# Kernel optimization log

Hardware: AMD Instinct MI355X
Metric: run time of the kernel (lower is better)

## Reference

```python
import jax, jax.numpy as jnp
import numpy as np
from math import sqrt

B, S, D_MODEL, H, DK, DV = 16, 512, 256, 8, 32, 32
EPS = 1e-5


def layer_norm(x, g, b):
    m = jnp.mean(x, axis=-1, keepdims=True)
    v = jnp.mean((x - m) ** 2, axis=-1, keepdims=True)
    return g * (x - m) / jnp.sqrt(v + EPS) + b


def setup_inputs() -> dict:
    key = jax.random.key(0)
    ks = jax.random.split(key, 16)
    inp = {
        "input_Q": jax.random.normal(ks[0], (B, S, D_MODEL), jnp.float32),
        "input_K": jax.random.normal(ks[1], (B, S, D_MODEL), jnp.float32),
        "input_V": jax.random.normal(ks[2], (B, S, D_MODEL), jnp.float32),
        "attn_mask": jax.random.bernoulli(ks[3], 0.1, (B, H, S, S)),
        "matrix": jax.random.uniform(ks[4], (B, S, S), jnp.float32),
        # learned params (stored [in, out], i.e. transpose of torch Linear weight)
        "W_Q": jax.random.normal(ks[5], (D_MODEL, H * DK), jnp.float32) * 0.02,
        "W_K": jax.random.normal(ks[6], (D_MODEL, H * DK), jnp.float32) * 0.02,
        "W_V": jax.random.normal(ks[7], (D_MODEL, H * DV), jnp.float32) * 0.02,
        "W_V2": jax.random.normal(ks[8], (D_MODEL, DV), jnp.float32) * 0.02,
        "W_fc": jax.random.normal(ks[9], (DV * (H + 1), D_MODEL), jnp.float32) * 0.02,
        "ln_g": jnp.ones((D_MODEL,), jnp.float32),
        "ln_b": jnp.zeros((D_MODEL,), jnp.float32),
        "fu_ln_g": jnp.ones((H + 1,), jnp.float32),
        "fu_ln_b": jnp.zeros((H + 1,), jnp.float32),
        "fu_w1": jax.random.normal(ks[10], (H + 1, 6), jnp.float32) * 0.3,
        "fu_b1": jnp.zeros((6,), jnp.float32),
        "fu_w2": jax.random.normal(ks[11], (6, 1), jnp.float32) * 0.3,
        "fu_b2": jnp.zeros((1,), jnp.float32),
    }
    return inp


def reference(input_Q, input_K, input_V, attn_mask, matrix,
              W_Q, W_K, W_V, W_V2, W_fc, ln_g, ln_b,
              fu_ln_g, fu_ln_b, fu_w1, fu_b1, fu_w2, fu_b2):
    b = input_Q.shape[0]
    # project and split heads: [B, H, S, d]
    Q = (input_Q @ W_Q).reshape(b, -1, H, DK).transpose(0, 2, 1, 3)
    K = (input_K @ W_K).reshape(b, -1, H, DK).transpose(0, 2, 1, 3)
    V = (input_V @ W_V).reshape(b, -1, H, DV).transpose(0, 2, 1, 3)
    scores = jnp.einsum('bhqd,bhkd->bhqk', Q, K) / sqrt(DK)
    scores = jnp.where(attn_mask, -1e9, scores)
    attn = jax.nn.softmax(scores, axis=-1)            # [B, H, S, S]
    context = jnp.einsum('bhqk,bhkd->bhqd', attn, V)  # [B, H, S, DV]
    # second context from pairwise matrix
    context2 = matrix @ (input_V @ W_V2)              # [B, S, DV]
    # gated matrix update: concat matrix with attn maps along head axis
    gate_in = jnp.concatenate([matrix[:, None], attn], axis=1)  # [B, H+1, S, S]
    gate_in = gate_in.transpose(0, 3, 2, 1)                     # [B, S, S, H+1]
    g = layer_norm(gate_in, fu_ln_g, fu_ln_b)
    g = jax.nn.relu(g @ fu_w1 + fu_b1)
    g = jax.nn.sigmoid(g @ fu_w2 + fu_b2)[..., 0]               # [B, S, S]
    matrix_out = matrix * g
    # merge heads, concat, project, layernorm
    context = context.transpose(0, 2, 1, 3).reshape(b, -1, H * DV)
    context = jnp.concatenate([context, context2], axis=-1)     # [B, S, DV*(H+1)]
    output = layer_norm(context @ W_fc, ln_g, ln_b)
    return (output, matrix_out)
```

## Files before the change

kernel.cpp:

```cpp
#include <hip/hip_runtime.h>
#include <hip/hip_bf16.h>

#define BB 16
#define SS 512
#define DM 256
#define NH 8

#define OFF_QB    0
#define OFF_KB    1048576
#define OFF_VT    2097152
#define OFF_VP2   3145728
#define OFF_CTXB  3407872
#define OFF_CTX2B 4456448
#define OFF_G     4587520
#define OFF_FLAG  6684672
#define OFF_PM    6684674

#define SCALE 0.17677669529663687f
#define KE2 0.2550348623f

typedef __attribute__((ext_vector_type(8))) short bfrag8;
typedef __attribute__((ext_vector_type(4))) float facc4;

__global__ void mask_or_kernel(const unsigned int* __restrict__ w,
                               unsigned int* __restrict__ acc) {
  __shared__ unsigned int sh[256];
  unsigned int a = 0;
  int base = blockIdx.x * 1024;
  for (int i = threadIdx.x; i < 1024; i += 256) a |= w[base + i];
  sh[threadIdx.x] = a;
  __syncthreads();
  for (int s = 128; s > 0; s >>= 1) {
    if (threadIdx.x < s) sh[threadIdx.x] |= sh[threadIdx.x + s];
    __syncthreads();
  }
  if (threadIdx.x == 0) atomicOr(acc, sh[0]);
}

__global__ __launch_bounds__(256) void mask_pack_kernel(
    const void* __restrict__ mask, unsigned long long* __restrict__ pm,
    const unsigned int* __restrict__ orv) {
  const unsigned int rawor = *orv;
  const int flagv = (rawor <= 1u) ? 0 : ((rawor == 0x3F800000u) ? 2 : 1);
  const int lane = threadIdx.x & 63;
  const int wv = threadIdx.x >> 6;
  const int w0 = (blockIdx.x * 4 + wv) * 32;
  const unsigned char* mb = (const unsigned char*)mask;
  const int* mi = (const int*)mask;
  const float* mf = (const float*)mask;
  unsigned long long myw = 0;
#pragma unroll 4
  for (int i = 0; i < 32; i++) {
    long long idx = (long long)(w0 + i) * 64 + lane;
    bool m;
    if (flagv == 1) m = (mb[idx] != 0);
    else if (flagv == 0) m = (mi[idx] != 0);
    else m = (mf[idx] != 0.f);
    unsigned long long bits = __ballot(m);
    if (lane == i) myw = bits;
  }
  if (lane < 32) pm[w0 + lane] = myw;
}

__global__ __launch_bounds__(256) void proj_pack_kernel(
    const float* __restrict__ inQ, const float* __restrict__ inK,
    const float* __restrict__ inV,
    const float* __restrict__ Wq, const float* __restrict__ Wk,
    const float* __restrict__ Wv, const float* __restrict__ Wv2,
    __hip_bfloat16* __restrict__ Qb, __hip_bfloat16* __restrict__ Kb,
    __hip_bfloat16* __restrict__ Vt, float* __restrict__ Vp2,
    const unsigned int* __restrict__ mask4,
    unsigned long long* __restrict__ pm) {
  __shared__ __align__(16) char smem[16640];
  const int tid = threadIdx.x;

  if (blockIdx.x < 1536) {
    auto As = reinterpret_cast<__hip_bfloat16(*)[40]>(smem);
    auto Bs = reinterpret_cast<__hip_bfloat16(*)[40]>(smem + 5120);
    const int bid = blockIdx.x;
    const int matid = bid >> 9;
    const int mblk = (bid & 511) >> 2;
    const int nblk = bid & 3;
    const int m0 = mblk * 64;
    const int n0 = nblk * 64;
    const float* X = (matid == 0) ? inQ : (matid == 1) ? inK : inV;
    const float* W = (matid == 0) ? Wq : (matid == 1) ? Wk : Wv;

    const int lane = tid & 63;
    const int w = tid >> 6;
    const int wm = w & 1, wn = w >> 1;
    const int cl = lane & 15, quad = lane >> 4;
    const int arow = tid >> 2, ak8 = (tid & 3) * 8;
    const int bn = tid & 63, bk8 = (tid >> 6) * 8;

    facc4 acc[2][2];
#pragma unroll
    for (int t = 0; t < 2; t++)
#pragma unroll
      for (int u = 0; u < 2; u++) acc[t][u] = (facc4){0.f, 0.f, 0.f, 0.f};

#pragma unroll 1
    for (int kc = 0; kc < 8; kc++) {
      float4 x0 = *(const float4*)&X[(m0 + arow) * 256 + kc * 32 + ak8];
      float4 x1 = *(const float4*)&X[(m0 + arow) * 256 + kc * 32 + ak8 + 4];
      float wv[8];
#pragma unroll
      for (int j = 0; j < 8; j++)
        wv[j] = W[(kc * 32 + bk8 + j) * 256 + n0 + bn];
      __syncthreads();
      {
        __hip_bfloat16 ta[8];
        ta[0] = __float2bfloat16(x0.x); ta[1] = __float2bfloat16(x0.y);
        ta[2] = __float2bfloat16(x0.z); ta[3] = __float2bfloat16(x0.w);
        ta[4] = __float2bfloat16(x1.x); ta[5] = __float2bfloat16(x1.y);
        ta[6] = __float2bfloat16(x1.z); ta[7] = __float2bfloat16(x1.w);
        *(uint4*)&As[arow][ak8] = *(uint4*)ta;
        __hip_bfloat16 tb[8];
#pragma unroll
        for (int j = 0; j < 8; j++) tb[j] = __float2bfloat16(wv[j]);
        *(uint4*)&Bs[bn][bk8] = *(uint4*)tb;
      }
      __syncthreads();
      bfrag8 aA[2], bB[2];
#pragma unroll
      for (int t = 0; t < 2; t++)
        aA[t] = *(const bfrag8*)&As[wm * 32 + t * 16 + cl][quad * 8];
#pragma unroll
      for (int u = 0; u < 2; u++)
        bB[u] = *(const bfrag8*)&Bs[wn * 32 + u * 16 + cl][quad * 8];
#pragma unroll
      for (int t = 0; t < 2; t++)
#pragma unroll
        for (int u = 0; u < 2; u++)
          acc[t][u] = __builtin_amdgcn_mfma_f32_16x16x32_bf16(aA[t], bB[u],
                                                             acc[t][u], 0, 0, 0);
    }

    if (matid < 2) {
      __hip_bfloat16* Y = (matid == 0) ? Qb : Kb;
#pragma unroll
      for (int t = 0; t < 2; t++)
#pragma unroll
        for (int u = 0; u < 2; u++)
#pragma unroll
          for (int reg = 0; reg < 4; reg++)
            Y[(m0 + wm * 32 + t * 16 + quad * 4 + reg) * 256 + n0 + wn * 32 +
              u * 16 + cl] = __float2bfloat16(acc[t][u][reg]);
    } else {
#pragma unroll
      for (int t = 0; t < 2; t++)
#pragma unroll
        for (int u = 0; u < 2; u++) {
          int c = n0 + wn * 32 + u * 16 + cl;
          int mg = m0 + wm * 32 + t * 16 + quad * 4;
          int b = mg >> 9, s = mg & 511;
          __hip_bfloat16 pk[4];
#pragma unroll
          for (int reg = 0; reg < 4; reg++)
            pk[reg] = __float2bfloat16(acc[t][u][reg]);
          *(ushort4*)&Vt[(((b << 8) + c) << 9) + s] = *(ushort4*)pk;
        }
    }
  } else if (blockIdx.x < 2048) {
    auto xs = reinterpret_cast<float(*)[260]>(smem);
    const int r0 = (blockIdx.x - 1536) * 16;
    for (int e = tid; e < 16 * 256; e += 256) {
      int r = e >> 8, i = e & 255;
      xs[r][i] = inV[(r0 + r) * 256 + i];
    }
    __syncthreads();
    const int c2 = tid & 31, rr = tid >> 5;
    float a0 = 0.f, a1 = 0.f;
    for (int i = 0; i < 256; i += 4) {
      float w0 = Wv2[i * 32 + c2], w1 = Wv2[(i + 1) * 32 + c2];
      float w2 = Wv2[(i + 2) * 32 + c2], w3 = Wv2[(i + 3) * 32 + c2];
      float4 xa = *(const float4*)&xs[rr][i];
      float4 xb = *(const float4*)&xs[rr + 8][i];
      a0 += xa.x * w0 + xa.y * w1 + xa.z * w2 + xa.w * w3;
      a1 += xb.x * w0 + xb.y * w1 + xb.z * w2 + xb.w * w3;
    }
    Vp2[(r0 + rr) * 32 + c2] = a0;
    Vp2[(r0 + rr + 8) * 32 + c2] = a1;
  } else {
    const int lane = tid & 63;
    const int wv = tid >> 6;
    const int w0 = ((blockIdx.x - 2048) * 4 + wv) * 32;
    unsigned long long myw = 0;
#pragma unroll 4
    for (int i = 0; i < 32; i++) {
      unsigned int v = mask4[(long long)(w0 + i) * 64 + lane];
      unsigned long long bits = __ballot(v != 0u);
      if (lane == i) myw = bits;
    }
    if (lane < 32) pm[w0 + lane] = myw;
  }
}

__global__ __launch_bounds__(512, 2) void attn_kernel(
    const __hip_bfloat16* __restrict__ Qb, const __hip_bfloat16* __restrict__ Kb,
    const __hip_bfloat16* __restrict__ Vt,
    const unsigned long long* __restrict__ pm,
    const float* __restrict__ matrix,
    const float* __restrict__ fulng, const float* __restrict__ fulnb,
    const float* __restrict__ fuw1, const float* __restrict__ fub1,
    const float* __restrict__ fuw2, const float* __restrict__ fub2,
    __hip_bfloat16* __restrict__ ctxb, __hip_bfloat16* __restrict__ gws) {
  __shared__ __align__(16) __hip_bfloat16 Sb[NH][16][520];
  __shared__ float inv_s[NH][16];
  __shared__ float gp[80];

  const int tid = threadIdx.x;
  const int lane = tid & 63;
  const int h = tid >> 6;
  const int cl = lane & 15, quad = lane >> 4;
  const int b = ((blockIdx.x & 7) << 1) | (blockIdx.x >> 8);
  const int q0 = ((blockIdx.x >> 3) & 31) * 16;

  if (tid < 6) {
    const int j = tid;
    float s1 = 0.f, c1 = fub1[j];
#pragma unroll
    for (int t = 0; t < 9; t++) {
      float w = fuw1[t * 6 + j];
      float gw = fulng[t] * w;
      gp[t * 6 + j] = gw;
      s1 += gw;
      c1 += fulnb[t] * w;
    }
    gp[54 + j] = s1;
    gp[60 + j] = c1;
    gp[66 + j] = fuw2[j];
    if (j == 0) gp[72] = fub2[0];
  }

  const unsigned long long* pmb = pm + (((b * NH + h) << 9) + q0) * 8;

  const bfrag8 aQ =
      *(const bfrag8*)&Qb[(((b << 9) + q0 + cl) << 8) + h * 32 + quad * 8];
  const __hip_bfloat16* KbB = &Kb[((b << 9) << 8) + h * 32 + quad * 8];
  const __hip_bfloat16* VtB = &Vt[(((b << 8) + h * 32) << 9)];

  float l[4] = {0.f, 0.f, 0.f, 0.f};
#pragma unroll 2
  for (int w8 = 0; w8 < 8; w8++) {
    unsigned long long mw[4];
#pragma unroll
    for (int r = 0; r < 4; r++)
      mw[r] = pmb[(quad * 4 + r) * 8 + w8] >> cl;
#pragma unroll
    for (int n4 = 0; n4 < 4; n4++) {
      const int nt = w8 * 4 + n4;
      bfrag8 bK = *(const bfrag8*)&KbB[(nt * 16 + cl) << 8];
      facc4 cc = {0.f, 0.f, 0.f, 0.f};
      cc = __builtin_amdgcn_mfma_f32_16x16x32_bf16(aQ, bK, cc, 0, 0, 0);
#pragma unroll
      for (int r = 0; r < 4; r++) {
        float e = ((mw[r] >> (n4 * 16)) & 1ULL) ? 0.f : exp2f(KE2 * cc[r]);
        l[r] += e;
        Sb[h][quad * 4 + r][nt * 16 + cl] = __float2bfloat16(e);
      }
    }
  }
#pragma unroll
  for (int r = 0; r < 4; r++)
#pragma unroll
    for (int off = 1; off <= 8; off <<= 1) l[r] += __shfl_xor(l[r], off);
  float invl[4];
#pragma unroll
  for (int r = 0; r < 4; r++) invl[r] = 1.f / l[r];
  if (cl == 0) {
#pragma unroll
    for (int r = 0; r < 4; r++) inv_s[h][quad * 4 + r] = invl[r];
  }
  __syncthreads();

  facc4 a0 = {0.f, 0.f, 0.f, 0.f}, a1 = {0.f, 0.f, 0.f, 0.f};
#pragma unroll 4
  for (int ks = 0; ks < 16; ks++) {
    bfrag8 aP = *(const bfrag8*)&Sb[h][cl][ks * 32 + quad * 8];
    bfrag8 b0 = *(const bfrag8*)&VtB[(cl << 9) + ks * 32 + quad * 8];
    bfrag8 b1 = *(const bfrag8*)&VtB[((16 + cl) << 9) + ks * 32 + quad * 8];
    a0 = __builtin_amdgcn_mfma_f32_16x16x32_bf16(aP, b0, a0, 0, 0, 0);
    a1 = __builtin_amdgcn_mfma_f32_16x16x32_bf16(aP, b1, a1, 0, 0, 0);
  }

  {
    const int gq = tid >> 5;
    const int g32 = (tid & 31) * 4;
#pragma unroll 1
    for (int s = 0; s < 4; s++) {
      const int k4 = s * 128 + g32;
      float4 mrow =
          *(const float4*)&matrix[((b << 9) + q0 + gq) * 512 + k4];
      float p[NH][4];
#pragma unroll
      for (int hh = 0; hh < NH; hh++) {
        const float iv = inv_s[hh][gq];
        ushort4 sv = *(const ushort4*)&Sb[hh][gq][k4];
        p[hh][0] = __bfloat162float(*(__hip_bfloat16*)&sv.x) * iv;
        p[hh][1] = __bfloat162float(*(__hip_bfloat16*)&sv.y) * iv;
        p[hh][2] = __bfloat162float(*(__hip_bfloat16*)&sv.z) * iv;
        p[hh][3] = __bfloat162float(*(__hip_bfloat16*)&sv.w) * iv;
      }
      const float mcomp[4] = {mrow.x, mrow.y, mrow.z, mrow.w};
      __hip_bfloat16 gout[4];
#pragma unroll
      for (int i = 0; i < 4; i++) {
        float v[9];
        v[0] = mcomp[i];
#pragma unroll
        for (int t = 0; t < NH; t++) v[1 + t] = p[t][i];
        float s1 = 0.f, s2 = 0.f;
#pragma unroll
        for (int t = 0; t < 9; t++) {
          s1 += v[t];
          s2 += v[t] * v[t];
        }
        float mu = s1 * (1.f / 9.f);
        float var = s2 * (1.f / 9.f) - mu * mu;
        float inv = rsqrtf(var + 1e-5f);
        float o = gp[72];
#pragma unroll
        for (int j = 0; j < 6; j++) {
          float d = 0.f;
#pragma unroll
          for (int t = 0; t < 9; t++) d += v[t] * gp[t * 6 + j];
          float z = inv * (d - mu * gp[54 + j]) + gp[60 + j];
          z = fmaxf(z, 0.f);
          o += z * gp[66 + j];
        }
        gout[i] = __float2bfloat16(1.f / (1.f + __expf(-o)));
      }
      *(ushort4*)&gws[((b << 9) + q0 + gq) * 512 + k4] = *(ushort4*)gout;
    }
  }

#pragma unroll
  for (int r = 0; r < 4; r++) {
    int row = quad * 4 + r;
    ctxb[((b << 9) + q0 + row) * 256 + h * 32 + cl] =
        __float2bfloat16(a0[r] * invl[r]);
    ctxb[((b << 9) + q0 + row) * 256 + h * 32 + 16 + cl] =
        __float2bfloat16(a1[r] * invl[r]);
  }
}

__global__ __launch_bounds__(256) void mout_ctx2_kernel(
    const float* __restrict__ matrix, const __hip_bfloat16* __restrict__ g,
    float* __restrict__ mout, const float* __restrict__ Vp2,
    __hip_bfloat16* __restrict__ ctx2b) {
  __shared__ __align__(16) char smem[25088];
  const int tid = threadIdx.x;

  if (blockIdx.x < 1024) {
    auto Gs = reinterpret_cast<float(*)[65]>(smem);
    const int b = blockIdx.x >> 6;
    const int j0 = ((blockIdx.x >> 3) & 7) * 64;
    const int i0 = (blockIdx.x & 7) * 64;

    {
      int r = tid >> 2, c0 = (tid & 3) * 16;
      const __hip_bfloat16* gpx = g + (((b << 9) + i0 + r) << 9) + j0 + c0;
      ushort us[16];
      *(uint4*)(us) = *(const uint4*)(gpx);
      *(uint4*)(us + 8) = *(const uint4*)(gpx + 8);
#pragma unroll
      for (int k = 0; k < 16; k++) {
        __hip_bfloat16 hv = *(__hip_bfloat16*)&us[k];
        Gs[r][c0 + k] = __bfloat162float(hv);
      }
    }
    __syncthreads();

    {
      int jj = tid >> 2, ic = (tid & 3) * 16;
      const float* mp = matrix + (((b << 9) + j0 + jj) << 9) + i0 + ic;
      float* op = mout + (((b << 9) + j0 + jj) << 9) + i0 + ic;
#pragma unroll
      for (int v4 = 0; v4 < 4; v4++) {
        float4 m = *(const float4*)(mp + v4 * 4);
        float4 o;
        o.x = m.x * Gs[ic + v4 * 4 + 0][jj];
        o.y = m.y * Gs[ic + v4 * 4 + 1][jj];
        o.z = m.z * Gs[ic + v4 * 4 + 2][jj];
        o.w = m.w * Gs[ic + v4 * 4 + 3][jj];
        *(float4*)(op + v4 * 4) = o;
      }
    }
  } else {
    auto Ms = reinterpret_cast<float(*)[128]>(smem);
    auto Vs2t = reinterpret_cast<float(*)[132]>(smem + 8192);
    const int cid = blockIdx.x - 1024;
    const int b = cid >> 5;
    const int s0 = (cid & 31) * 16;
    const int dv = tid & 31, rg = tid >> 5;
    float acc0 = 0.f, acc1 = 0.f;
    for (int kc = 0; kc < 4; kc++) {
      __syncthreads();
#pragma unroll
      for (int it = 0; it < 8; it++) {
        int idx = tid + it * 256;
        int r = idx >> 7, cc = idx & 127;
        Ms[r][cc] = matrix[((b << 9) + s0 + r) * 512 + kc * 128 + cc];
      }
#pragma unroll
      for (int it = 0; it < 16; it++) {
        int e = tid + it * 256;
        int k = e >> 5, dv2 = e & 31;
        Vs2t[dv2][k] = Vp2[((b << 9) + kc * 128 + k) * 32 + dv2];
      }
      __syncthreads();
      for (int k = 0; k < 128; k += 4) {
        float4 vv = *(const float4*)&Vs2t[dv][k];
        float4 m0 = *(const float4*)&Ms[rg][k];
        float4 m1 = *(const float4*)&Ms[rg + 8][k];
        acc0 += m0.x * vv.x + m0.y * vv.y + m0.z * vv.z + m0.w * vv.w;
        acc1 += m1.x * vv.x + m1.y * vv.y + m1.z * vv.z + m1.w * vv.w;
      }
    }
    ctx2b[((b << 9) + s0 + rg) * 32 + dv] = __float2bfloat16(acc0);
    ctx2b[((b << 9) + s0 + rg + 8) * 32 + dv] = __float2bfloat16(acc1);
  }
}

__global__ __launch_bounds__(256) void final_kernel(
    const __hip_bfloat16* __restrict__ ctxb,
    const __hip_bfloat16* __restrict__ ctx2b, const float* __restrict__ Wfc,
    const float* __restrict__ lng, const float* __restrict__ lnb,
    float* __restrict__ out) {
  __shared__ __align__(16) __hip_bfloat16 As[32][40];
  __shared__ __align__(16) __hip_bfloat16 Bs[256][40];
  __shared__ __align__(16) float xs[32][260];
  __shared__ float red2[32][8][2];
  __shared__ float musig[32][2];
  const int tid = threadIdx.x;
  const int m0 = blockIdx.x * 32;
  const int lane = tid & 63, w = tid >> 6;
  const int cl = lane & 15, quad = lane >> 4;
  const int arow = tid >> 3, ak4 = (tid & 7) * 4;

  facc4 acc[2][4];
#pragma unroll
  for (int t = 0; t < 2; t++)
#pragma unroll
    for (int u = 0; u < 4; u++) acc[t][u] = (facc4){0.f, 0.f, 0.f, 0.f};

#pragma unroll 1
  for (int kc = 0; kc < 9; kc++) {
    ushort4 av;
    if (kc < 8)
      av = *(const ushort4*)&ctxb[(m0 + arow) * 256 + kc * 32 + ak4];
    else
      av = *(const ushort4*)&ctx2b[(m0 + arow) * 32 + ak4];
    float wv[32];
#pragma unroll
    for (int j = 0; j < 32; j++) wv[j] = Wfc[(kc * 32 + j) * 256 + tid];
    __syncthreads();
    *(ushort4*)&As[arow][ak4] = av;
    {
      __hip_bfloat16 tw[32];
#pragma unroll
      for (int j = 0; j < 32; j++) tw[j] = __float2bfloat16(wv[j]);
#pragma unroll
      for (int g = 0; g < 4; g++) *(uint4*)&Bs[tid][g * 8] = *(uint4*)&tw[g * 8];
    }
    __syncthreads();
    bfrag8 aA[2], bB[4];
#pragma unroll
    for (int t = 0; t < 2; t++)
      aA[t] = *(const bfrag8*)&As[t * 16 + cl][quad * 8];
#pragma unroll
    for (int u = 0; u < 4; u++)
      bB[u] = *(const bfrag8*)&Bs[w * 64 + u * 16 + cl][quad * 8];
#pragma unroll
    for (int t = 0; t < 2; t++)
#pragma unroll
      for (int u = 0; u < 4; u++)
        acc[t][u] =
            __builtin_amdgcn_mfma_f32_16x16x32_bf16(aA[t], bB[u], acc[t][u], 0, 0, 0);
  }

#pragma unroll
  for (int t = 0; t < 2; t++)
#pragma unroll
    for (int u = 0; u < 4; u++)
#pragma unroll
      for (int reg = 0; reg < 4; reg++)
        xs[t * 16 + quad * 4 + reg][w * 64 + u * 16 + cl] = acc[t][u][reg];
  __syncthreads();

  {
    int r = tid >> 3, c0 = (tid & 7) * 32;
    float s1 = 0.f, s2 = 0.f;
    for (int j = 0; j < 32; j += 4) {
      float4 v = *(const float4*)&xs[r][c0 + j];
      s1 += v.x + v.y + v.z + v.w;
      s2 += v.x * v.x + v.y * v.y + v.z * v.z + v.w * v.w;
    }
    red2[r][tid & 7][0] = s1;
    red2[r][tid & 7][1] = s2;
  }
  __syncthreads();
  if (tid < 32) {
    float s1 = 0.f, s2 = 0.f;
#pragma unroll
    for (int j = 0; j < 8; j++) {
      s1 += red2[tid][j][0];
      s2 += red2[tid][j][1];
    }
    float mu = s1 * (1.f / 256.f);
    float var = s2 * (1.f / 256.f) - mu * mu;
    musig[tid][0] = mu;
    musig[tid][1] = rsqrtf(var + 1e-5f);
  }
  __syncthreads();
  {
    float gt = lng[tid], bt = lnb[tid];
#pragma unroll 4
    for (int r = 0; r < 32; r++)
      out[(m0 + r) * 256 + tid] =
          gt * (xs[r][tid] - musig[r][0]) * musig[r][1] + bt;
  }
}

extern "C" void kernel_launch(void* const* d_in, const int* in_sizes, int n_in,
                              void* d_out, int out_size, void* d_ws,
                              size_t ws_size, hipStream_t stream) {
  const float* inQ = (const float*)d_in[0];
  const float* inK = (const float*)d_in[1];
  const float* inV = (const float*)d_in[2];
  const void* mask = d_in[3];
  const float* matrix = (const float*)d_in[4];
  const float* Wq = (const float*)d_in[5];
  const float* Wk = (const float*)d_in[6];
  const float* Wv = (const float*)d_in[7];
  const float* Wv2 = (const float*)d_in[8];
  const float* Wfc = (const float*)d_in[9];
  const float* lng = (const float*)d_in[10];
  const float* lnb = (const float*)d_in[11];
  const float* fulng = (const float*)d_in[12];
  const float* fulnb = (const float*)d_in[13];
  const float* fuw1 = (const float*)d_in[14];
  const float* fub1 = (const float*)d_in[15];
  const float* fuw2 = (const float*)d_in[16];
  const float* fub2 = (const float*)d_in[17];

  float* ws = (float*)d_ws;
  __hip_bfloat16* Qb = (__hip_bfloat16*)(ws + OFF_QB);
  __hip_bfloat16* Kb = (__hip_bfloat16*)(ws + OFF_KB);
  __hip_bfloat16* Vt = (__hip_bfloat16*)(ws + OFF_VT);
  float* Vp2 = ws + OFF_VP2;
  __hip_bfloat16* ctxb = (__hip_bfloat16*)(ws + OFF_CTXB);
  __hip_bfloat16* ctx2b = (__hip_bfloat16*)(ws + OFF_CTX2B);
  __hip_bfloat16* gws = (__hip_bfloat16*)(ws + OFF_G);
  unsigned int* flag = (unsigned int*)(ws + OFF_FLAG);
  unsigned long long* pmask = (unsigned long long*)(ws + OFF_PM);

  float* out = (float*)d_out;
  float* mout = out + BB * SS * DM;

  const long long MASKN = (long long)BB * NH * SS * SS;
  if (in_sizes[3] == (int)(MASKN * 4)) {
    proj_pack_kernel<<<6144, 256, 0, stream>>>(
        inQ, inK, inV, Wq, Wk, Wv, Wv2, Qb, Kb, Vt, Vp2,
        (const unsigned int*)mask, pmask);
  } else {
    hipMemsetAsync(flag, 0, 4, stream);
    mask_or_kernel<<<64, 256, 0, stream>>>((const unsigned int*)mask, flag);
    mask_pack_kernel<<<4096, 256, 0, stream>>>(mask, pmask, flag);
    proj_pack_kernel<<<2048, 256, 0, stream>>>(
        inQ, inK, inV, Wq, Wk, Wv, Wv2, Qb, Kb, Vt, Vp2,
        (const unsigned int*)mask, pmask);
  }
  attn_kernel<<<512, 512, 0, stream>>>(Qb, Kb, Vt, pmask, matrix, fulng, fulnb,
                                       fuw1, fub1, fuw2, fub2, ctxb, gws);
  mout_ctx2_kernel<<<1536, 256, 0, stream>>>(matrix, gws, mout, Vp2, ctx2b);
  final_kernel<<<256, 256, 0, stream>>>(ctxb, ctx2b, Wfc, lng, lnb, out);
}
```

Baseline: 379.8 us.

## Halve attention LDS score buffer by recomputing second key half

The attention kernel now keeps only half of the score row in shared memory (256 keys instead of 512). The first pass computes exponentials for the first half and stores them. For the second half it computes only the row sums, then later recomputes QK^T and the exponentials to fill the buffer again. Halving the buffer lets launch bounds request 4 blocks per CU instead of 2 to raise occupancy. In exchange, half of the QK^T MFMAs and exponentials run twice, and two extra block-wide barriers are added.

```diff
diff --git a/kernel.cpp b/kernel.cpp
--- a/kernel.cpp
+++ b/kernel.cpp
@@ -196,7 +196,7 @@
   }
 }
 
-__global__ __launch_bounds__(512, 2) void attn_kernel(
+__global__ __launch_bounds__(512, 4) void attn_kernel(
     const __hip_bfloat16* __restrict__ Qb, const __hip_bfloat16* __restrict__ Kb,
     const __hip_bfloat16* __restrict__ Vt,
     const unsigned long long* __restrict__ pm,
@@ -205,7 +205,7 @@
     const float* __restrict__ fuw1, const float* __restrict__ fub1,
     const float* __restrict__ fuw2, const float* __restrict__ fub2,
     __hip_bfloat16* __restrict__ ctxb, __hip_bfloat16* __restrict__ gws) {
-  __shared__ __align__(16) __hip_bfloat16 Sb[NH][16][520];
+  __shared__ __align__(16) __hip_bfloat16 Sb[NH][16][264];
   __shared__ float inv_s[NH][16];
   __shared__ float gp[80];
 
@@ -242,7 +242,7 @@
 
   float l[4] = {0.f, 0.f, 0.f, 0.f};
 #pragma unroll 2
-  for (int w8 = 0; w8 < 8; w8++) {
+  for (int w8 = 0; w8 < 4; w8++) {
     unsigned long long mw[4];
 #pragma unroll
     for (int r = 0; r < 4; r++)
@@ -261,6 +261,25 @@
       }
     }
   }
+#pragma unroll 2
+  for (int w8 = 4; w8 < 8; w8++) {
+    unsigned long long mw[4];
+#pragma unroll
+    for (int r = 0; r < 4; r++)
+      mw[r] = pmb[(quad * 4 + r) * 8 + w8] >> cl;
+#pragma unroll
+    for (int n4 = 0; n4 < 4; n4++) {
+      const int nt = w8 * 4 + n4;
+      bfrag8 bK = *(const bfrag8*)&KbB[(nt * 16 + cl) << 8];
+      facc4 cc = {0.f, 0.f, 0.f, 0.f};
+      cc = __builtin_amdgcn_mfma_f32_16x16x32_bf16(aQ, bK, cc, 0, 0, 0);
+#pragma unroll
+      for (int r = 0; r < 4; r++) {
+        float e = ((mw[r] >> (n4 * 16)) & 1ULL) ? 0.f : exp2f(KE2 * cc[r]);
+        l[r] += e;
+      }
+    }
+  }
 #pragma unroll
   for (int r = 0; r < 4; r++)
 #pragma unroll
@@ -276,63 +295,136 @@
 
   facc4 a0 = {0.f, 0.f, 0.f, 0.f}, a1 = {0.f, 0.f, 0.f, 0.f};
 #pragma unroll 4
-  for (int ks = 0; ks < 16; ks++) {
+  for (int ks = 0; ks < 8; ks++) {
     bfrag8 aP = *(const bfrag8*)&Sb[h][cl][ks * 32 + quad * 8];
     bfrag8 b0 = *(const bfrag8*)&VtB[(cl << 9) + ks * 32 + quad * 8];
     bfrag8 b1 = *(const bfrag8*)&VtB[((16 + cl) << 9) + ks * 32 + quad * 8];
     a0 = __builtin_amdgcn_mfma_f32_16x16x32_bf16(aP, b0, a0, 0, 0, 0);
     a1 = __builtin_amdgcn_mfma_f32_16x16x32_bf16(aP, b1, a1, 0, 0, 0);
   }
-
-  {
-    const int gq = tid >> 5;
-    const int g32 = (tid & 31) * 4;
+  const int gq = tid >> 5;
+  const int g32 = (tid & 31) * 4;
 #pragma unroll 1
-    for (int s = 0; s < 4; s++) {
-      const int k4 = s * 128 + g32;
-      float4 mrow =
-          *(const float4*)&matrix[((b << 9) + q0 + gq) * 512 + k4];
-      float p[NH][4];
-#pragma unroll
-      for (int hh = 0; hh < NH; hh++) {
-        const float iv = inv_s[hh][gq];
-        ushort4 sv = *(const ushort4*)&Sb[hh][gq][k4];
-        p[hh][0] = __bfloat162float(*(__hip_bfloat16*)&sv.x) * iv;
-        p[hh][1] = __bfloat162float(*(__hip_bfloat16*)&sv.y) * iv;
-        p[hh][2] = __bfloat162float(*(__hip_bfloat16*)&sv.z) * iv;
-        p[hh][3] = __bfloat162float(*(__hip_bfloat16*)&sv.w) * iv;
-      }
-      const float mcomp[4] = {mrow.x, mrow.y, mrow.z, mrow.w};
-      __hip_bfloat16 gout[4];
-#pragma unroll
-      for (int i = 0; i < 4; i++) {
-        float v[9];
-        v[0] = mcomp[i];
-#pragma unroll
-        for (int t = 0; t < NH; t++) v[1 + t] = p[t][i];
-        float s1 = 0.f, s2 = 0.f;
-#pragma unroll
-        for (int t = 0; t < 9; t++) {
-          s1 += v[t];
-          s2 += v[t] * v[t];
-        }
-        float mu = s1 * (1.f / 9.f);
-        float var = s2 * (1.f / 9.f) - mu * mu;
-        float inv = rsqrtf(var + 1e-5f);
-        float o = gp[72];
-#pragma unroll
-        for (int j = 0; j < 6; j++) {
-          float d = 0.f;
-#pragma unroll
-          for (int t = 0; t < 9; t++) d += v[t] * gp[t * 6 + j];
-          float z = inv * (d - mu * gp[54 + j]) + gp[60 + j];
-          z = fmaxf(z, 0.f);
-          o += z * gp[66 + j];
-        }
-        gout[i] = __float2bfloat16(1.f / (1.f + __expf(-o)));
-      }
-      *(ushort4*)&gws[((b << 9) + q0 + gq) * 512 + k4] = *(ushort4*)gout;
-    }
+  for (int s = 0; s < 2; s++) {
+    const int k4 = s * 128 + g32;
+    float4 mrow = *(const float4*)&matrix[((b << 9) + q0 + gq) * 512 + k4];
+    float p[NH][4];
+#pragma unroll
+    for (int hh = 0; hh < NH; hh++) {
+      const float iv = inv_s[hh][gq];
+      ushort4 sv = *(const ushort4*)&Sb[hh][gq][k4];
+      p[hh][0] = __bfloat162float(*(__hip_bfloat16*)&sv.x) * iv;
+      p[hh][1] = __bfloat162float(*(__hip_bfloat16*)&sv.y) * iv;
+      p[hh][2] = __bfloat162float(*(__hip_bfloat16*)&sv.z) * iv;
+      p[hh][3] = __bfloat162float(*(__hip_bfloat16*)&sv.w) * iv;
+    }
+    const float mcomp[4] = {mrow.x, mrow.y, mrow.z, mrow.w};
+    __hip_bfloat16 gout[4];
+#pragma unroll
+    for (int i = 0; i < 4; i++) {
+      float v[9];
+      v[0] = mcomp[i];
+#pragma unroll
+      for (int t = 0; t < NH; t++) v[1 + t] = p[t][i];
+      float s1 = 0.f, s2 = 0.f;
+#pragma unroll
+      for (int t = 0; t < 9; t++) {
+        s1 += v[t];
+        s2 += v[t] * v[t];
+      }
+      float mu = s1 * (1.f / 9.f);
+      float var = s2 * (1.f / 9.f) - mu * mu;
+      float inv = rsqrtf(var + 1e-5f);
+      float o = gp[72];
+#pragma unroll
+      for (int j = 0; j < 6; j++) {
+        float d = 0.f;
+#pragma unroll
+        for (int t = 0; t < 9; t++) d += v[t] * gp[t * 6 + j];
+        float z = inv * (d - mu * gp[54 + j]) + gp[60 + j];
+        z = fmaxf(z, 0.f);
+        o += z * gp[66 + j];
+      }
+      gout[i] = __float2bfloat16(1.f / (1.f + __expf(-o)));
+    }
+    *(ushort4*)&gws[((b << 9) + q0 + gq) * 512 + k4] = *(ushort4*)gout;
+  }
+  __syncthreads();
+
+#pragma unroll 2
+  for (int w8 = 4; w8 < 8; w8++) {
+    unsigned long long mw[4];
+#pragma unroll
+    for (int r = 0; r < 4; r++)
+      mw[r] = pmb[(quad * 4 + r) * 8 + w8] >> cl;
+#pragma unroll
+    for (int n4 = 0; n4 < 4; n4++) {
+      const int nt = w8 * 4 + n4;
+      bfrag8 bK = *(const bfrag8*)&KbB[(nt * 16 + cl) << 8];
+      facc4 cc = {0.f, 0.f, 0.f, 0.f};
+      cc = __builtin_amdgcn_mfma_f32_16x16x32_bf16(aQ, bK, cc, 0, 0, 0);
+#pragma unroll
+      for (int r = 0; r < 4; r++) {
+        float e = ((mw[r] >> (n4 * 16)) & 1ULL) ? 0.f : exp2f(KE2 * cc[r]);
+        Sb[h][quad * 4 + r][(nt - 16) * 16 + cl] = __float2bfloat16(e);
+      }
+    }
+  }
+  __syncthreads();
+
+#pragma unroll 4
+  for (int ks = 8; ks < 16; ks++) {
+    bfrag8 aP = *(const bfrag8*)&Sb[h][cl][(ks - 8) * 32 + quad * 8];
+    bfrag8 b0 = *(const bfrag8*)&VtB[(cl << 9) + ks * 32 + quad * 8];
+    bfrag8 b1 = *(const bfrag8*)&VtB[((16 + cl) << 9) + ks * 32 + quad * 8];
+    a0 = __builtin_amdgcn_mfma_f32_16x16x32_bf16(aP, b0, a0, 0, 0, 0);
+    a1 = __builtin_amdgcn_mfma_f32_16x16x32_bf16(aP, b1, a1, 0, 0, 0);
+  }
+#pragma unroll 1
+  for (int s = 2; s < 4; s++) {
+    const int k4 = s * 128 + g32;
+    const int lc = k4 - 256;
+    float4 mrow = *(const float4*)&matrix[((b << 9) + q0 + gq) * 512 + k4];
+    float p[NH][4];
+#pragma unroll
+    for (int hh = 0; hh < NH; hh++) {
+      const float iv = inv_s[hh][gq];
+      ushort4 sv = *(const ushort4*)&Sb[hh][gq][lc];
+      p[hh][0] = __bfloat162float(*(__hip_bfloat16*)&sv.x) * iv;
+      p[hh][1] = __bfloat162float(*(__hip_bfloat16*)&sv.y) * iv;
+      p[hh][2] = __bfloat162float(*(__hip_bfloat16*)&sv.z) * iv;
+      p[hh][3] = __bfloat162float(*(__hip_bfloat16*)&sv.w) * iv;
+    }
+    const float mcomp[4] = {mrow.x, mrow.y, mrow.z, mrow.w};
+    __hip_bfloat16 gout[4];
+#pragma unroll
+    for (int i = 0; i < 4; i++) {
+      float v[9];
+      v[0] = mcomp[i];
+#pragma unroll
+      for (int t = 0; t < NH; t++) v[1 + t] = p[t][i];
+      float s1 = 0.f, s2 = 0.f;
+#pragma unroll
+      for (int t = 0; t < 9; t++) {
+        s1 += v[t];
+        s2 += v[t] * v[t];
+      }
+      float mu = s1 * (1.f / 9.f);
+      float var = s2 * (1.f / 9.f) - mu * mu;
+      float inv = rsqrtf(var + 1e-5f);
+      float o = gp[72];
+#pragma unroll
+      for (int j = 0; j < 6; j++) {
+        float d = 0.f;
+#pragma unroll
+        for (int t = 0; t < 9; t++) d += v[t] * gp[t * 6 + j];
+        float z = inv * (d - mu * gp[54 + j]) + gp[60 + j];
+        z = fmaxf(z, 0.f);
+        o += z * gp[66 + j];
+      }
+      gout[i] = __float2bfloat16(1.f / (1.f + __expf(-o)));
+    }
+    *(ushort4*)&gws[((b << 9) + q0 + gq) * 512 + k4] = *(ushort4*)gout;
   }
 
 #pragma unroll
```

Measured after the change: 397.4 us. 1.05x slower.
